# Kernel optimization log

Hardware: AMD Instinct MI355X
Metric: run time of the kernel (lower is better)

Reference implementation:

```python
import jax, jax.numpy as jnp
import numpy as np

WARMUP_EPOCHS = 5
RAMP_EPOCHS = 40
SCRATCH_CLIP = 5.0
THETA_MAX = 5.0
LN_EPS = 1e-5


def _leaky(v):
    return jnp.where(v > 0, v, 0.01 * v)


def setup_inputs() -> dict:
    key = jax.random.key(0)
    ks = jax.random.split(key, 16)
    B, T, F, E, H, G = 1024, 256, 64, 256, 256, 32
    s = lambda k, *sh: jax.random.normal(k, sh, dtype=jnp.float32) * 0.05
    return {
        "obs": jax.random.normal(ks[0], (B, T, F), dtype=jnp.float32),
        "h0": jnp.zeros((B, H), dtype=jnp.float32),
        "epoch": 100,
        "obs_W": s(ks[1], F, E), "obs_b": jnp.zeros((E,), jnp.float32),
        "enc_W": s(ks[2], E, E), "enc_b": jnp.zeros((E,), jnp.float32),
        "pre_W": s(ks[3], E, E), "pre_b": jnp.zeros((E,), jnp.float32),
        "pred_W": s(ks[4], H, H), "pred_b": jnp.zeros((H,), jnp.float32),
        "Wrz_W": s(ks[5], E + H, 2 * H), "Wrz_b": jnp.zeros((2 * H,), jnp.float32),
        "Wn_W": s(ks[6], E + H, H), "Wn_b": jnp.zeros((H,), jnp.float32),
        "g1_W": s(ks[7], H, G), "g1_b": jnp.zeros((G,), jnp.float32),
        "ln_g": jnp.ones((G,), jnp.float32), "ln_b": jnp.zeros((G,), jnp.float32),
        "g2_W": s(ks[8], G, G), "g2_b": jnp.zeros((G,), jnp.float32),
        "g3_W": s(ks[9], G, 3 * H), "g3_b": jnp.zeros((3 * H,), jnp.float32),
        "dp_W": s(ks[10], H, H),
    }


def reference(obs, h0, epoch, obs_W, obs_b, enc_W, enc_b, pre_W, pre_b,
              pred_W, pred_b, Wrz_W, Wrz_b, Wn_W, Wn_b,
              g1_W, g1_b, ln_g, ln_b, g2_W, g2_b, g3_W, g3_b, dp_W):
    H = h0.shape[-1]
    # DenseEncoder (vector mode): Linear -> LayerNorm(no affine) -> Linear -> LeakyReLU
    e = obs @ obs_W + obs_b                                # (B,T,E)
    mu = e.mean(-1, keepdims=True)
    var = ((e - mu) ** 2).mean(-1, keepdims=True)
    e = (e - mu) * jax.lax.rsqrt(var + LN_EPS)
    e = _leaky(e @ enc_W + enc_b)
    # policy preprocessor: Linear -> LeakyReLU
    x = _leaky(e @ pre_W + pre_b)                          # (B,T,E)

    # surprise ramp (epoch is static python int)
    if epoch < WARMUP_EPOCHS:
        scale = 0.0
    else:
        scale = min(1.0, (epoch - WARMUP_EPOCHS) / RAMP_EPOCHS)

    def step(h, x_t):
        # surprise = prediction error of the belief predictor
        delta = (h @ pred_W + pred_b) - h                  # (B,H)
        cat = jnp.concatenate([x_t, h], axis=-1)
        rz = jax.nn.sigmoid(cat @ Wrz_W + Wrz_b)
        r, z = rz[:, :H], rz[:, H:]
        n = jnp.tanh(jnp.concatenate([x_t, r * h], axis=-1) @ Wn_W + Wn_b)
        # gate_net: Linear -> LN(affine) -> ReLU -> (Dropout eval=id) -> Linear -> ReLU -> Linear
        g = delta @ g1_W + g1_b
        gmu = g.mean(-1, keepdims=True)
        gvar = ((g - gmu) ** 2).mean(-1, keepdims=True)
        g = (g - gmu) * jax.lax.rsqrt(gvar + LN_EPS) * ln_g + ln_b
        g = jax.nn.relu(g)
        g = jax.nn.relu(g @ g2_W + g2_b)
        g = g @ g3_W + g3_b                                # (B,3H)
        eta = jax.nn.sigmoid(g[:, :H])
        theta = jnp.minimum(jax.nn.softplus(g[:, H:2 * H]), THETA_MAX)
        alpha = jax.nn.sigmoid(g[:, 2 * H:]) * scale
        delta_h = delta @ dp_W
        s_t = jnp.clip(eta * h - theta * delta_h, -SCRATCH_CLIP, SCRATCH_CLIP)
        h_tilde = (1 - alpha) * h + alpha * s_t
        h_new = z * h_tilde + (1 - z) * n
        return h_new, h_new

    _, hs = jax.lax.scan(step, h0, jnp.swapaxes(x, 0, 1))  # (T,B,H)
    return jnp.swapaxes(hs, 0, 1)                          # (B,T,H)
```

## Files before the change

kernel.cpp:

```cpp
#include <hip/hip_runtime.h>

typedef __bf16 bf16;
typedef __bf16 bf16x8 __attribute__((ext_vector_type(8)));
typedef float  f32x4  __attribute__((ext_vector_type(4)));
typedef unsigned int       u32;
typedef unsigned short     u16;
typedef unsigned long long u64;

__device__ __forceinline__ f32x4 mfma16(bf16x8 a, bf16x8 b, f32x4 c) {
  return __builtin_amdgcn_mfma_f32_16x16x32_bf16(a, b, c, 0, 0, 0);
}
__device__ __forceinline__ float sigm(float x)  { return 1.0f / (1.0f + __expf(-x)); }
__device__ __forceinline__ float tanh_(float x) { return 2.0f / (1.0f + __expf(-2.0f * x)) - 1.0f; }
__device__ __forceinline__ float softplus_(float x) {
  return fmaxf(x, 0.0f) + __logf(1.0f + __expf(-fabsf(x)));
}
__device__ __forceinline__ float leaky_(float x) { return x > 0.0f ? x : 0.01f * x; }
__device__ __forceinline__ u16 bfbits(float f) { return __builtin_bit_cast(u16, (bf16)f); }


__global__ void k_transpose(const float* __restrict__ src, bf16* __restrict__ dst, int K, int N) {
  int i = blockIdx.x * 256 + threadIdx.x;
  if (i < K * N) { int k = i / N; int n = i - k * N; dst[n * K + k] = (bf16)src[i]; }
}

__global__ void k_p2(const float* __restrict__ pred, const float* __restrict__ dp, bf16* __restrict__ P2T) {
  int i = blockIdx.x * 256 + threadIdx.x;
  int irow = i >> 8, n = i & 255;
  float acc = 0.0f;
  for (int j = 0; j < 256; ++j) {
    float p = pred[irow * 256 + j] - (j == irow ? 1.0f : 0.0f);
    acc += p * dp[j * 256 + n];
  }
  P2T[n * 256 + irow] = (bf16)acc;
}

__global__ void k_p1(const float* __restrict__ pred, const float* __restrict__ g1, bf16* __restrict__ P1T) {
  int i = blockIdx.x * 256 + threadIdx.x;
  int irow = i >> 5, n = i & 31;
  float acc = 0.0f;
  for (int j = 0; j < 256; ++j) {
    float p = pred[irow * 256 + j] - (j == irow ? 1.0f : 0.0f);
    acc += p * g1[j * 32 + n];
  }
  P1T[n * 256 + irow] = (bf16)acc;
}

__global__ void k_cvec(const float* __restrict__ pred_b, const float* __restrict__ dp,
                       const float* __restrict__ g1, const float* __restrict__ g1_b,
                       float* __restrict__ c2f, float* __restrict__ c1f) {
  int n = threadIdx.x;
  float acc = 0.0f;
  for (int j = 0; j < 256; ++j) acc += pred_b[j] * dp[j * 256 + n];
  c2f[n] = acc;
  if (n < 32) {
    float a2 = 0.0f;
    for (int j = 0; j < 256; ++j) a2 += pred_b[j] * g1[j * 32 + n];
    c1f[n] = a2 + g1_b[n];
  }
}

__global__ void k_zero(u32* __restrict__ p, int n) {
  int i = blockIdx.x * 256 + threadIdx.x;
  if (i < n) p[i] = 0;
}


__global__ __launch_bounds__(256, 2) void k_phase1(
    const float* __restrict__ obs,
    const bf16* __restrict__ obs_WT, const bf16* __restrict__ enc_WT, const bf16* __restrict__ pre_WT,
    const float* __restrict__ obs_b, const float* __restrict__ enc_b, const float* __restrict__ pre_b,
    float* __restrict__ out)
{
  const int tid  = threadIdx.x;
  const int lane = tid & 63;
  const int w    = tid >> 6;
  const int n16  = lane & 15, quad = lane >> 4;
  const long R0  = (long)blockIdx.x * 64;

  __shared__ __align__(16) bf16 obsb[64][72];
  __shared__ __align__(16) bf16 ebuf[64][264];
  __shared__ __align__(16) bf16 e2buf[64][264];
  __shared__ float red[64][8];

  {
    int row = tid >> 2, col = (tid & 3) * 16;
    const float* src = obs + (R0 + row) * 64 + col;
    #pragma unroll
    for (int q = 0; q < 16; ++q) obsb[row][col + q] = (bf16)src[q];
  }
  __syncthreads();

  {
    f32x4 acc[4][4] = {};
    #pragma unroll
    for (int ks = 0; ks < 2; ++ks) {
      bf16x8 a[4];
      #pragma unroll
      for (int mt = 0; mt < 4; ++mt) a[mt] = *(const bf16x8*)&obsb[mt * 16 + n16][ks * 32 + quad * 8];
      #pragma unroll
      for (int nt = 0; nt < 4; ++nt) {
        int ncol = (4 * w + nt) * 16 + n16;
        bf16x8 b = *(const bf16x8*)(obs_WT + ncol * 64 + ks * 32 + quad * 8);
        #pragma unroll
        for (int mt = 0; mt < 4; ++mt) acc[mt][nt] = mfma16(a[mt], b, acc[mt][nt]);
      }
    }
    #pragma unroll
    for (int nt = 0; nt < 4; ++nt) {
      int ncol = (4 * w + nt) * 16 + n16;
      float bb = obs_b[ncol];
      #pragma unroll
      for (int mt = 0; mt < 4; ++mt)
        #pragma unroll
        for (int reg = 0; reg < 4; ++reg)
          ebuf[mt * 16 + quad * 4 + reg][ncol] = (bf16)(acc[mt][nt][reg] + bb);
    }
  }
  __syncthreads();
  {
    int row = tid >> 2, qt = tid & 3;
    float s = 0, s2 = 0;
    for (int c = 0; c < 64; ++c) { float v = (float)ebuf[row][qt * 64 + c]; s += v; s2 += v * v; }
    red[row][qt] = s; red[row][4 + qt] = s2;
  }
  __syncthreads();
  if (tid < 64) {
    float s  = red[tid][0] + red[tid][1] + red[tid][2] + red[tid][3];
    float s2 = red[tid][4] + red[tid][5] + red[tid][6] + red[tid][7];
    float mu = s * (1.0f / 256.0f);
    float var = s2 * (1.0f / 256.0f) - mu * mu;
    red[tid][0] = mu; red[tid][1] = rsqrtf(var + 1e-5f);
  }
  __syncthreads();
  {
    int row = tid >> 2, qt = tid & 3;
    float mu = red[row][0], rstd = red[row][1];
    for (int c = 0; c < 64; ++c) {
      int cc = qt * 64 + c;
      ebuf[row][cc] = (bf16)(((float)ebuf[row][cc] - mu) * rstd);
    }
  }
  __syncthreads();
  {
    f32x4 acc[4][4] = {};
    #pragma unroll
    for (int ks = 0; ks < 8; ++ks) {
      bf16x8 a[4];
      #pragma unroll
      for (int mt = 0; mt < 4; ++mt) a[mt] = *(const bf16x8*)&ebuf[mt * 16 + n16][ks * 32 + quad * 8];
      #pragma unroll
      for (int nt = 0; nt < 4; ++nt) {
        int ncol = (4 * w + nt) * 16 + n16;
        bf16x8 b = *(const bf16x8*)(enc_WT + ncol * 256 + ks * 32 + quad * 8);
        #pragma unroll
        for (int mt = 0; mt < 4; ++mt) acc[mt][nt] = mfma16(a[mt], b, acc[mt][nt]);
      }
    }
    #pragma unroll
    for (int nt = 0; nt < 4; ++nt) {
      int ncol = (4 * w + nt) * 16 + n16;
      float bb = enc_b[ncol];
      #pragma unroll
      for (int mt = 0; mt < 4; ++mt)
        #pragma unroll
        for (int reg = 0; reg < 4; ++reg)
          e2buf[mt * 16 + quad * 4 + reg][ncol] = (bf16)leaky_(acc[mt][nt][reg] + bb);
    }
  }
  __syncthreads();
  {
    f32x4 acc[4][4] = {};
    #pragma unroll
    for (int ks = 0; ks < 8; ++ks) {
      bf16x8 a[4];
      #pragma unroll
      for (int mt = 0; mt < 4; ++mt) a[mt] = *(const bf16x8*)&e2buf[mt * 16 + n16][ks * 32 + quad * 8];
      #pragma unroll
      for (int nt = 0; nt < 4; ++nt) {
        int ncol = (4 * w + nt) * 16 + n16;
        bf16x8 b = *(const bf16x8*)(pre_WT + ncol * 256 + ks * 32 + quad * 8);
        #pragma unroll
        for (int mt = 0; mt < 4; ++mt) acc[mt][nt] = mfma16(a[mt], b, acc[mt][nt]);
      }
    }
    #pragma unroll
    for (int nt = 0; nt < 4; ++nt) {
      int ncol = (4 * w + nt) * 16 + n16;
      float bb = pre_b[ncol];
      #pragma unroll
      for (int mt = 0; mt < 4; ++mt)
        #pragma unroll
        for (int reg = 0; reg < 4; ++reg)
          out[(R0 + mt * 16 + quad * 4 + reg) * 256 + ncol] = leaky_(acc[mt][nt][reg] + bb);
    }
  }
}


__global__ __launch_bounds__(512, 1) void k_phase2(
    const float* __restrict__ h0,
    const int*  __restrict__ epoch_p,
    float* __restrict__ out,
    const bf16* __restrict__ WrzT, const bf16* __restrict__ WnT,
    const bf16* __restrict__ P2T,  const bf16* __restrict__ P1T,
    const bf16* __restrict__ g2T,  const bf16* __restrict__ g3T,
    const float* __restrict__ c2f, const float* __restrict__ c1f,
    const float* __restrict__ Wrz_b, const float* __restrict__ Wn_b,
    const float* __restrict__ g2_b,  const float* __restrict__ g3_b,
    const float* __restrict__ ln_g,  const float* __restrict__ ln_b,
    u64* __restrict__ rhx, u32* __restrict__ rhflag, u32* __restrict__ hflag)
{
  const int tid  = threadIdx.x;
  const int lane = tid & 63;
  const int w    = tid >> 6;
  const int wlow = w & 3;
  const int hi   = w >> 2;
  const int n16  = lane & 15;
  const int quad = lane >> 4;
  const int g    = blockIdx.x >> 2;
  const int q    = blockIdx.x & 3;
  const int b0   = g * 16;
  const int c    = q * 64 + wlow * 16 + n16;

  __shared__ __align__(16) bf16  Abuf[16][520];
  __shared__ __align__(16) float gbuf[16][36];
  __shared__ __align__(16) bf16  gact[16][40];
  __shared__ __align__(16) bf16  g2act[16][40];
  __shared__ float red[4][64][17];
  __shared__ float lngs[32], lnbs[32];

  if (tid < 32) { lngs[tid] = ln_g[tid]; lnbs[tid] = ln_b[tid]; }

  const int ep = *epoch_p;
  const float scale = fminf(1.0f, fmaxf(0.0f, ((float)ep - 5.0f) / 40.0f));

  const float brz_r = Wrz_b[c];
  const float brz_z = Wrz_b[256 + c];
  const float bwn   = Wn_b[c];
  const float bg3e  = g3_b[c];
  const float bg3t  = g3_b[256 + c];
  const float bg3a  = g3_b[512 + c];
  const float c2v   = c2f[c];
  const float c1v   = (wlow < 2) ? c1f[wlow * 16 + n16] : 0.0f;
  const float g2bv0 = g2_b[n16];
  const float g2bv1 = g2_b[16 + n16];

  float hreg[4];
  #pragma unroll
  for (int r = 0; r < 4; ++r)
    hreg[r] = h0[(long)(b0 + quad * 4 + r) * 256 + c];

  const int srow = tid >> 5;
  const int scol = (tid & 31) * 8;

  {
    const float* hp = h0 + (long)(b0 + srow) * 256 + scol;
    const float* xp = out + ((long)(b0 + srow) * 256 + 0) * 256 + scol;
    bf16x8 xv, hv;
    #pragma unroll
    for (int j = 0; j < 8; ++j) { xv[j] = (bf16)xp[j]; hv[j] = (bf16)hp[j]; }
    *(bf16x8*)&Abuf[srow][scol]       = xv;
    *(bf16x8*)&Abuf[srow][256 + scol] = hv;
  }
  __syncthreads();

  const bf16* Ab = &Abuf[n16][quad * 8];
  u32* rhF = rhflag + g * 16;
  u32* hF  = hflag  + g * 16;
  const int k0 = hi * 4;

  for (int t = 0; t < 256; ++t) {
    const bool notlast = (t < 255);

    f32x4 xr0 = {}, xr1 = {};
    if (notlast) {
      const float* xp = out + ((long)(b0 + srow) * 256 + (t + 1)) * 256 + scol;
      xr0 = *(const f32x4*)(xp);
      xr1 = *(const f32x4*)(xp + 4);
    }

    f32x4 accr = {}, accz = {}, accn = {}, accdh = {}, accg = {};
    #pragma unroll
    for (int ks = 0; ks < 4; ++ks) {
      const int kk = k0 + ks;
      bf16x8 a = *(const bf16x8*)(Ab + kk * 32);
      const bf16* bp = WrzT + (long)c * 512 + kk * 32 + quad * 8;
      accr = mfma16(a, *(const bf16x8*)(bp),             accr);
      accz = mfma16(a, *(const bf16x8*)(bp + 256 * 512), accz);
      accn = mfma16(a, *(const bf16x8*)(WnT + (long)c * 512 + kk * 32 + quad * 8), accn);
    }

    if (t > 0 && tid == 320) {
      const u32 tgt = 4u * (u32)t;
      while (__hip_atomic_load(hF, __ATOMIC_RELAXED, __HIP_MEMORY_SCOPE_AGENT) < tgt) {}
    }
    __syncthreads();
    if (t > 0) {
      const u64* hp = (const u64*)(out + ((long)(b0 + srow) * 256 + (t - 1)) * 256 + scol);
      bf16x8 o;
      #pragma unroll
      for (int j = 0; j < 4; ++j) {
        u64 v = __hip_atomic_load(hp + j, __ATOMIC_RELAXED, __HIP_MEMORY_SCOPE_AGENT);
        o[2 * j]     = (bf16)__builtin_bit_cast(float, (u32)(v & 0xffffffffull));
        o[2 * j + 1] = (bf16)__builtin_bit_cast(float, (u32)(v >> 32));
      }
      *(bf16x8*)&Abuf[srow][256 + scol] = o;
    }
    if (notlast) {
      bf16x8 v;
      #pragma unroll
      for (int j = 0; j < 4; ++j) { v[j] = (bf16)xr0[j]; v[4 + j] = (bf16)xr1[j]; }
      *(bf16x8*)&Abuf[srow][scol] = v;
    }
    __syncthreads();

    #pragma unroll
    for (int ks = 0; ks < 4; ++ks) {
      const int kk = 8 + k0 + ks;
      bf16x8 a = *(const bf16x8*)(Ab + kk * 32);
      const bf16* bp = WrzT + (long)c * 512 + kk * 32 + quad * 8;
      accr = mfma16(a, *(const bf16x8*)(bp),             accr);
      accz = mfma16(a, *(const bf16x8*)(bp + 256 * 512), accz);
    }
    #pragma unroll
    for (int ks = 0; ks < 4; ++ks) {
      const int kk = k0 + ks;
      bf16x8 a = *(const bf16x8*)(Ab + 256 + kk * 32);
      accdh = mfma16(a, *(const bf16x8*)(P2T + (long)c * 256 + kk * 32 + quad * 8), accdh);
      if (wlow < 2)
        accg = mfma16(a, *(const bf16x8*)(P1T + (wlow * 16 + n16) * 256 + kk * 32 + quad * 8), accg);
    }

    if (hi) {
      #pragma unroll
      for (int r = 0; r < 4; ++r) red[wlow][lane][r] = accr[r];
      if (wlow < 2) {
        #pragma unroll
        for (int r = 0; r < 4; ++r) red[wlow][lane][4 + r] = accg[r];
      }
    }
    __syncthreads();

    if (!hi) {
      u64 pk = 0;
      #pragma unroll
      for (int r = 0; r < 4; ++r) {
        float rv = sigm(accr[r] + red[wlow][lane][r] + brz_r);
        pk |= (u64)bfbits(rv * hreg[r]) << (16 * r);
      }
      __hip_atomic_store(rhx + ((long)(g * 256 + c)) * 4 + quad, pk,
                         __ATOMIC_RELAXED, __HIP_MEMORY_SCOPE_AGENT);
      if (wlow < 2) {
        #pragma unroll
        for (int r = 0; r < 4; ++r)
          gbuf[quad * 4 + r][wlow * 16 + n16] = accg[r] + red[wlow][lane][4 + r] + c1v;
      }
    }
    asm volatile("s_waitcnt vmcnt(0)" ::: "memory");
    __syncthreads();
    if (tid == 256)
      __hip_atomic_fetch_add(rhF, 1u, __ATOMIC_RELAXED, __HIP_MEMORY_SCOPE_AGENT);

    if (tid < 16) {
      float mu = 0, s2 = 0;
      #pragma unroll
      for (int cc = 0; cc < 32; ++cc) { float v = gbuf[tid][cc]; mu += v; s2 += v * v; }
      mu *= (1.0f / 32.0f);
      s2 = s2 * (1.0f / 32.0f) - mu * mu;
      float rstd = rsqrtf(s2 + 1e-5f);
      #pragma unroll
      for (int cc = 0; cc < 32; ++cc) {
        float gn = (gbuf[tid][cc] - mu) * rstd * lngs[cc] + lnbs[cc];
        gact[tid][cc] = (bf16)fmaxf(gn, 0.0f);
      }
    }
    __syncthreads();
    if (w == 0) {
      bf16x8 a = *(const bf16x8*)&gact[n16][quad * 8];
      f32x4 a0 = {}, a1 = {};
      a0 = mfma16(a, *(const bf16x8*)(g2T + n16 * 32 + quad * 8), a0);
      a1 = mfma16(a, *(const bf16x8*)(g2T + (16 + n16) * 32 + quad * 8), a1);
      #pragma unroll
      for (int r = 0; r < 4; ++r) {
        int row = quad * 4 + r;
        g2act[row][n16]      = (bf16)fmaxf(a0[r] + g2bv0, 0.0f);
        g2act[row][16 + n16] = (bf16)fmaxf(a1[r] + g2bv1, 0.0f);
      }
    }
    if (tid == 320) {
      const u32 tgt = 4u * (u32)(t + 1);
      while (__hip_atomic_load(rhF, __ATOMIC_RELAXED, __HIP_MEMORY_SCOPE_AGENT) < tgt) {}
    }
    __syncthreads();

    {
      const int cc = tid >> 1;
      const int jb = (tid & 1) * 2;
      const u64* rp = rhx + ((long)(g * 256 + cc)) * 4 + jb;
      #pragma unroll
      for (int jj = 0; jj < 2; ++jj) {
        u64 v = __hip_atomic_load(rp + jj, __ATOMIC_RELAXED, __HIP_MEMORY_SCOPE_AGENT);
        #pragma unroll
        for (int r = 0; r < 4; ++r)
          *(u16*)&Abuf[(jb + jj) * 4 + r][256 + cc] = (u16)(v >> (16 * r));
      }
    }
    __syncthreads();

    #pragma unroll
    for (int ks = 0; ks < 4; ++ks) {
      const int kk = 8 + k0 + ks;
      bf16x8 a = *(const bf16x8*)(Ab + kk * 32);
      accn = mfma16(a, *(const bf16x8*)(WnT + (long)c * 512 + kk * 32 + quad * 8), accn);
    }
    f32x4 acce = {}, acct = {}, acca = {};
    if (!hi) {
      bf16x8 a3 = *(const bf16x8*)&g2act[n16][quad * 8];
      const bf16* bp3 = g3T + (long)c * 32 + quad * 8;
      acce = mfma16(a3, *(const bf16x8*)(bp3),            acce);
      acct = mfma16(a3, *(const bf16x8*)(bp3 + 256 * 32), acct);
      acca = mfma16(a3, *(const bf16x8*)(bp3 + 512 * 32), acca);
    }
    if (hi) {
      #pragma unroll
      for (int r = 0; r < 4; ++r) {
        red[wlow][lane][r]     = accz[r];
        red[wlow][lane][4 + r] = accdh[r];
        red[wlow][lane][8 + r] = accn[r];
      }
    }
    __syncthreads();

    if (!hi) {
      float* op = out + ((long)(b0 + quad * 4) * 256 + t) * 256 + c;
      #pragma unroll
      for (int r = 0; r < 4; ++r) {
        float hv  = hreg[r];
        float zf  = sigm(accz[r] + red[wlow][lane][r] + brz_z);
        float dh  = accdh[r] + red[wlow][lane][4 + r] + c2v;
        float nn  = tanh_(accn[r] + red[wlow][lane][8 + r] + bwn);
        float eta = sigm(acce[r] + bg3e);
        float th  = fminf(softplus_(acct[r] + bg3t), 5.0f);
        float al  = sigm(acca[r] + bg3a) * scale;
        float s   = fminf(fmaxf(eta * hv - th * dh, -5.0f), 5.0f);
        float htl = (1.0f - al) * hv + al * s;
        float hn  = zf * htl + (1.0f - zf) * nn;
        hreg[r] = hn;
        __hip_atomic_store(op + (long)r * 65536, hn,
                           __ATOMIC_RELAXED, __HIP_MEMORY_SCOPE_AGENT);
      }
    }
    asm volatile("s_waitcnt vmcnt(0)" ::: "memory");
    __syncthreads();
    if (tid == 256 && notlast)
      __hip_atomic_fetch_add(hF, 1u, __ATOMIC_RELAXED, __HIP_MEMORY_SCOPE_AGENT);
  }
}


extern "C" void kernel_launch(void* const* d_in, const int* in_sizes, int n_in,
                              void* d_out, int out_size, void* d_ws, size_t ws_size,
                              hipStream_t stream) {
  const float* obs    = (const float*)d_in[0];
  const float* h0     = (const float*)d_in[1];
  const int*   epoch  = (const int*)  d_in[2];
  const float* obs_W  = (const float*)d_in[3];
  const float* obs_b  = (const float*)d_in[4];
  const float* enc_W  = (const float*)d_in[5];
  const float* enc_b  = (const float*)d_in[6];
  const float* pre_W  = (const float*)d_in[7];
  const float* pre_b  = (const float*)d_in[8];
  const float* pred_W = (const float*)d_in[9];
  const float* pred_b = (const float*)d_in[10];
  const float* Wrz_W  = (const float*)d_in[11];
  const float* Wrz_b  = (const float*)d_in[12];
  const float* Wn_W   = (const float*)d_in[13];
  const float* Wn_b   = (const float*)d_in[14];
  const float* g1_W   = (const float*)d_in[15];
  const float* g1_b   = (const float*)d_in[16];
  const float* ln_g   = (const float*)d_in[17];
  const float* ln_b   = (const float*)d_in[18];
  const float* g2_W   = (const float*)d_in[19];
  const float* g2_b   = (const float*)d_in[20];
  const float* g3_W   = (const float*)d_in[21];
  const float* g3_b   = (const float*)d_in[22];
  const float* dp_W   = (const float*)d_in[23];

  bf16* W = (bf16*)d_ws;
  bf16* WrzT  = W + 0;
  bf16* WnT   = W + 262144;
  bf16* P2T   = W + 393216;
  bf16* P1T   = W + 458752;
  bf16* g2T   = W + 466944;
  bf16* g3T   = W + 467968;
  bf16* obsWT = W + 492544;
  bf16* encWT = W + 508928;
  bf16* preWT = W + 574464;
  float* c2f  = (float*)((char*)d_ws + 1280000);
  float* c1f  = (float*)((char*)d_ws + 1281024);
  u64*  rhx   = (u64*) ((char*)d_ws + 1281152);
  u32*  rhfl  = (u32*) ((char*)d_ws + 1805440);
  u32*  hfl   = (u32*) ((char*)d_ws + 1809536);
  float* out = (float*)d_out;

  k_zero<<<8, 256, 0, stream>>>(rhfl, 2048);

  k_transpose<<<1024, 256, 0, stream>>>(Wrz_W, WrzT, 512, 512);
  k_transpose<<<512,  256, 0, stream>>>(Wn_W,  WnT,  512, 256);
  k_transpose<<<4,    256, 0, stream>>>(g2_W,  g2T,  32,  32);
  k_transpose<<<96,   256, 0, stream>>>(g3_W,  g3T,  32,  768);
  k_transpose<<<64,   256, 0, stream>>>(obs_W, obsWT, 64, 256);
  k_transpose<<<256,  256, 0, stream>>>(enc_W, encWT, 256, 256);
  k_transpose<<<256,  256, 0, stream>>>(pre_W, preWT, 256, 256);
  k_p2<<<256, 256, 0, stream>>>(pred_W, dp_W, P2T);
  k_p1<<<32,  256, 0, stream>>>(pred_W, g1_W, P1T);
  k_cvec<<<1, 256, 0, stream>>>(pred_b, dp_W, g1_W, g1_b, c2f, c1f);

  k_phase1<<<4096, 256, 0, stream>>>(obs, obsWT, encWT, preWT, obs_b, enc_b, pre_b, out);
  k_phase2<<<256, 512, 0, stream>>>(h0, epoch, out, WrzT, WnT, P2T, P1T, g2T, g3T,
                                    c2f, c1f, Wrz_b, Wn_b, g2_b, g3_b, ln_g, ln_b,
                                    rhx, rhfl, hfl);

  (void)in_sizes; (void)n_in; (void)out_size; (void)ws_size;
}
```

Baseline: 2.369 ms.

## Keep recurrent GRU weights in registers and gate/predictor weights in LDS

The serial-scan kernel now loads each wave's slices of the Wrz and Wn weights into registers once, before the timestep loop. The P2, P1, g2 and g3 weight tiles are staged into shared memory once, so the 256-step loop no longer re-reads weights from global memory or L2 on every step. The launch-bounds occupancy hint is raised from 1 to 2. In exchange the kernel holds 24 extra bf16x8 values per thread, which raises register pressure and risks spills, and it uses considerably more LDS.

Result: faster. 2.126 ms (-10.3%).

```diff
diff --git a/kernel.cpp b/kernel.cpp
--- a/kernel.cpp
+++ b/kernel.cpp
@@ -198,7 +198,7 @@
 }
 
 
-__global__ __launch_bounds__(512, 1) void k_phase2(
+__global__ __launch_bounds__(512, 2) void k_phase2(
     const float* __restrict__ h0,
     const int*  __restrict__ epoch_p,
     float* __restrict__ out,
@@ -221,7 +221,8 @@
   const int g    = blockIdx.x >> 2;
   const int q    = blockIdx.x & 3;
   const int b0   = g * 16;
-  const int c    = q * 64 + wlow * 16 + n16;
+  const int lc   = wlow * 16 + n16;
+  const int c    = q * 64 + lc;
 
   __shared__ __align__(16) bf16  Abuf[16][520];
   __shared__ __align__(16) float gbuf[16][36];
@@ -229,6 +230,10 @@
   __shared__ __align__(16) bf16  g2act[16][40];
   __shared__ float red[4][64][17];
   __shared__ float lngs[32], lnbs[32];
+  __shared__ __align__(16) bf16 P2L[64 * 264];
+  __shared__ __align__(16) bf16 P1L[32 * 264];
+  __shared__ __align__(16) bf16 g3L[3 * 64 * 40];
+  __shared__ __align__(16) bf16 g2L[1024];
 
   if (tid < 32) { lngs[tid] = ln_g[tid]; lnbs[tid] = ln_b[tid]; }
 
@@ -246,6 +251,37 @@
   const float g2bv0 = g2_b[n16];
   const float g2bv1 = g2_b[16 + n16];
 
+  const int k0 = hi * 4;
+
+  bf16x8 Br[8], Bz[8], Bn[8];
+  {
+    const bf16* wrz = WrzT + (long)c * 512 + quad * 8;
+    const bf16* wn  = WnT  + (long)c * 512 + quad * 8;
+    #pragma unroll
+    for (int i = 0; i < 4; ++i) {
+      Br[i]     = *(const bf16x8*)(wrz + (k0 + i) * 32);
+      Br[4 + i] = *(const bf16x8*)(wrz + (8 + k0 + i) * 32);
+      Bz[i]     = *(const bf16x8*)(wrz + 256 * 512 + (k0 + i) * 32);
+      Bz[4 + i] = *(const bf16x8*)(wrz + 256 * 512 + (8 + k0 + i) * 32);
+      Bn[i]     = *(const bf16x8*)(wn + (k0 + i) * 32);
+      Bn[4 + i] = *(const bf16x8*)(wn + (8 + k0 + i) * 32);
+    }
+  }
+  for (int i = tid; i < 2048; i += 512) {
+    int col = i >> 5, ch = i & 31;
+    *(bf16x8*)&P2L[col * 264 + ch * 8] = *(const bf16x8*)(P2T + (long)(q * 64 + col) * 256 + ch * 8);
+  }
+  for (int i = tid; i < 1024; i += 512) {
+    int col = i >> 5, ch = i & 31;
+    *(bf16x8*)&P1L[col * 264 + ch * 8] = *(const bf16x8*)(P1T + (long)col * 256 + ch * 8);
+  }
+  for (int i = tid; i < 768; i += 512) {
+    int s = i >> 8, col = (i >> 2) & 63, ch = i & 3;
+    *(bf16x8*)&g3L[(s * 64 + col) * 40 + ch * 8] = *(const bf16x8*)(g3T + (long)(s * 256 + q * 64 + col) * 32 + ch * 8);
+  }
+  for (int i = tid; i < 128; i += 512)
+    *(bf16x8*)&g2L[i * 8] = *(const bf16x8*)(g2T + i * 8);
+
   float hreg[4];
   #pragma unroll
   for (int r = 0; r < 4; ++r)
@@ -268,7 +304,6 @@
   const bf16* Ab = &Abuf[n16][quad * 8];
   u32* rhF = rhflag + g * 16;
   u32* hF  = hflag  + g * 16;
-  const int k0 = hi * 4;
 
   for (int t = 0; t < 256; ++t) {
     const bool notlast = (t < 255);
@@ -283,12 +318,10 @@
     f32x4 accr = {}, accz = {}, accn = {}, accdh = {}, accg = {};
     #pragma unroll
     for (int ks = 0; ks < 4; ++ks) {
-      const int kk = k0 + ks;
-      bf16x8 a = *(const bf16x8*)(Ab + kk * 32);
-      const bf16* bp = WrzT + (long)c * 512 + kk * 32 + quad * 8;
-      accr = mfma16(a, *(const bf16x8*)(bp),             accr);
-      accz = mfma16(a, *(const bf16x8*)(bp + 256 * 512), accz);
-      accn = mfma16(a, *(const bf16x8*)(WnT + (long)c * 512 + kk * 32 + quad * 8), accn);
+      bf16x8 a = *(const bf16x8*)(Ab + (k0 + ks) * 32);
+      accr = mfma16(a, Br[ks], accr);
+      accz = mfma16(a, Bz[ks], accz);
+      accn = mfma16(a, Bn[ks], accn);
     }
 
     if (t > 0 && tid == 320) {
@@ -317,19 +350,17 @@
 
     #pragma unroll
     for (int ks = 0; ks < 4; ++ks) {
-      const int kk = 8 + k0 + ks;
-      bf16x8 a = *(const bf16x8*)(Ab + kk * 32);
-      const bf16* bp = WrzT + (long)c * 512 + kk * 32 + quad * 8;
-      accr = mfma16(a, *(const bf16x8*)(bp),             accr);
-      accz = mfma16(a, *(const bf16x8*)(bp + 256 * 512), accz);
+      bf16x8 a = *(const bf16x8*)(Ab + (8 + k0 + ks) * 32);
+      accr = mfma16(a, Br[4 + ks], accr);
+      accz = mfma16(a, Bz[4 + ks], accz);
     }
     #pragma unroll
     for (int ks = 0; ks < 4; ++ks) {
       const int kk = k0 + ks;
       bf16x8 a = *(const bf16x8*)(Ab + 256 + kk * 32);
-      accdh = mfma16(a, *(const bf16x8*)(P2T + (long)c * 256 + kk * 32 + quad * 8), accdh);
+      accdh = mfma16(a, *(const bf16x8*)&P2L[lc * 264 + kk * 32 + quad * 8], accdh);
       if (wlow < 2)
-        accg = mfma16(a, *(const bf16x8*)(P1T + (wlow * 16 + n16) * 256 + kk * 32 + quad * 8), accg);
+        accg = mfma16(a, *(const bf16x8*)&P1L[(wlow * 16 + n16) * 264 + kk * 32 + quad * 8], accg);
     }
 
     if (hi) {
@@ -379,8 +410,8 @@
     if (w == 0) {
       bf16x8 a = *(const bf16x8*)&gact[n16][quad * 8];
       f32x4 a0 = {}, a1 = {};
-      a0 = mfma16(a, *(const bf16x8*)(g2T + n16 * 32 + quad * 8), a0);
-      a1 = mfma16(a, *(const bf16x8*)(g2T + (16 + n16) * 32 + quad * 8), a1);
+      a0 = mfma16(a, *(const bf16x8*)&g2L[n16 * 32 + quad * 8], a0);
+      a1 = mfma16(a, *(const bf16x8*)&g2L[(16 + n16) * 32 + quad * 8], a1);
       #pragma unroll
       for (int r = 0; r < 4; ++r) {
         int row = quad * 4 + r;
@@ -410,17 +441,15 @@
 
     #pragma unroll
     for (int ks = 0; ks < 4; ++ks) {
-      const int kk = 8 + k0 + ks;
-      bf16x8 a = *(const bf16x8*)(Ab + kk * 32);
-      accn = mfma16(a, *(const bf16x8*)(WnT + (long)c * 512 + kk * 32 + quad * 8), accn);
+      bf16x8 a = *(const bf16x8*)(Ab + (8 + k0 + ks) * 32);
+      accn = mfma16(a, Bn[4 + ks], accn);
     }
     f32x4 acce = {}, acct = {}, acca = {};
     if (!hi) {
       bf16x8 a3 = *(const bf16x8*)&g2act[n16][quad * 8];
-      const bf16* bp3 = g3T + (long)c * 32 + quad * 8;
-      acce = mfma16(a3, *(const bf16x8*)(bp3),            acce);
-      acct = mfma16(a3, *(const bf16x8*)(bp3 + 256 * 32), acct);
-      acca = mfma16(a3, *(const bf16x8*)(bp3 + 512 * 32), acca);
+      acce = mfma16(a3, *(const bf16x8*)&g3L[(0 * 64 + lc) * 40 + quad * 8], acce);
+      acct = mfma16(a3, *(const bf16x8*)&g3L[(1 * 64 + lc) * 40 + quad * 8], acct);
+      acca = mfma16(a3, *(const bf16x8*)&g3L[(2 * 64 + lc) * 40 + quad * 8], acca);
     }
     if (hi) {
       #pragma unroll
```
